# Performance work log

Hardware: AMD Instinct MI355X
Metric: run time of the kernel (lower is better)

The kernel has to match this reference:

```python
import jax, jax.numpy as jnp
import numpy as np

N_HEAD = 8
N_FEAT = 256
CHUNK = 64          # window/chunk size N
D_K = N_FEAT // N_HEAD
SCALE = D_K ** (-0.5)
B_ = 2048           # batch * nChunkNum
NCHUNK = 128        # nChunkNum (B_ % NCHUNK == 0)


def setup_inputs() -> dict:
    key = jax.random.key(0)
    ks = jax.random.split(key, 12)
    f32 = jnp.float32
    query = jax.random.normal(ks[0], (B_, CHUNK, N_FEAT), f32)
    key_t = jax.random.normal(ks[1], (B_, CHUNK, N_FEAT), f32)
    value = jax.random.normal(ks[2], (B_, CHUNK, N_FEAT), f32)
    # padding mask (B_, time2): multiplicative 0/1 floats
    mask = jax.random.randint(ks[3], (B_, CHUNK), 0, 2).astype(f32)
    # shifted-chunk additive mask (nChunkNum, N, N): 0 for neighbors, -100 otherwise
    cm_bin = jax.random.randint(ks[4], (NCHUNK, CHUNK, CHUNK), 0, 2)
    chunk_mask = jnp.where(cm_bin == 1, 0.0, -100.0).astype(f32)
    def lin(k):
        return jax.random.normal(k, (N_FEAT, N_FEAT), f32) * 0.02
    Wq, Wk, Wv, Wo = lin(ks[5]), lin(ks[6]), lin(ks[7]), lin(ks[8])
    bq = jnp.zeros((N_FEAT,), f32)
    bk = jnp.zeros((N_FEAT,), f32)
    bv = jnp.zeros((N_FEAT,), f32)
    bo = jnp.zeros((N_FEAT,), f32)
    rpb_table = jax.random.normal(ks[9], (2 * CHUNK - 1, N_HEAD), f32) * 0.02
    return {"query": query, "key": key_t, "value": value, "mask": mask,
            "chunk_mask": chunk_mask, "Wq": Wq, "bq": bq, "Wk": Wk, "bk": bk,
            "Wv": Wv, "bv": bv, "Wo": Wo, "bo": bo, "rpb_table": rpb_table}


def _rel_pos_index():
    # index[i, j] = (i - j) + CHUNK - 1, shape (N, N)
    w = jnp.arange(CHUNK)
    return w[:, None] - w[None, :] + (CHUNK - 1)


def reference(query, key, value, mask, chunk_mask, Wq, bq, Wk, bk, Wv, bv, Wo, bo, rpb_table):
    B, N, _ = query.shape
    # qkv projections -> (B, h, N, d_k)
    def proj(x, W, b):
        y = x @ W.T + b
        return y.reshape(B, N, N_HEAD, D_K).transpose(0, 2, 1, 3)
    q = proj(query, Wq, bq)
    k = proj(key, Wk, bk)
    v = proj(value, Wv, bv)
    # windowed attention scores (B, h, N, N)
    scores = jnp.einsum("bhid,bhjd->bhij", q, k) * SCALE
    # relative position bias: gather (N, N, h) -> (h, N, N)
    rpb = rpb_table[_rel_pos_index()].transpose(2, 0, 1)
    scores = scores + rpb[None]
    # padding mask: multiply, then fill zeros with -100 (as in torch source)
    scores = scores * mask[:, None, None, :]
    scores = jnp.where(scores == 0, jnp.float32(-100.0), scores)
    # additive shifted-chunk mask
    nC = chunk_mask.shape[0]
    scores = scores.reshape(B // nC, nC, N_HEAD, N, N) + chunk_mask[None, :, None]
    scores = scores.reshape(B, N_HEAD, N, N)
    attn = jax.nn.softmax(scores, axis=-1)
    x = jnp.einsum("bhij,bhjd->bhid", attn, v)          # (B, h, N, d_k)
    x = x.transpose(0, 2, 1, 3).reshape(B, N, N_FEAT)     # (B, N, n_feat)
    return x @ Wo.T + bo
```

## Files before the change

kernel.cpp:

```cpp
#include <hip/hip_runtime.h>
#include <hip/hip_bf16.h>

typedef __bf16 bf16_t;
typedef __bf16 bf16x8 __attribute__((ext_vector_type(8)));
typedef __bf16 bf16x4 __attribute__((ext_vector_type(4)));
typedef float f32x4 __attribute__((ext_vector_type(4)));

#define LDA 264
#define SMEM_BYTES 142560

#define OFF_X   0
#define OFF_K   33792
#define OFF_Q   67584
#define OFF_VT  101376
#define OFF_RPB 138240
#define OFF_MSK 142304

__device__ __forceinline__ void stage_x(const float* __restrict__ src, bf16_t* __restrict__ dst, int tid) {
  const float4* s4 = (const float4*)src;
#pragma unroll
  for (int k = 0; k < 8; ++k) {
    int f = tid + (k << 9);
    float4 v = s4[f];
    int row = f >> 6;
    int col = (f & 63) << 2;
    bf16x4 p;
    p[0] = (bf16_t)v.x; p[1] = (bf16_t)v.y; p[2] = (bf16_t)v.z; p[3] = (bf16_t)v.w;
    *(bf16x4*)(dst + row*LDA + col) = p;
  }
}

__device__ __forceinline__ void gemm_64x32(const bf16_t* __restrict__ A, const bf16_t* __restrict__ W,
                                           int cb, int l15, int g, f32x4 acc[4][2]) {
#pragma unroll
  for (int kt = 0; kt < 8; ++kt) {
    bf16x8 a[4];
#pragma unroll
    for (int mt = 0; mt < 4; ++mt)
      a[mt] = *(const bf16x8*)(A + (mt*16 + l15)*LDA + kt*32 + g*8);
#pragma unroll
    for (int nt = 0; nt < 2; ++nt) {
      bf16x8 bw = *(const bf16x8*)(W + (cb + nt*16 + l15)*256 + kt*32 + g*8);
#pragma unroll
      for (int mt = 0; mt < 4; ++mt)
        acc[mt][nt] = __builtin_amdgcn_mfma_f32_16x16x32_bf16(a[mt], bw, acc[mt][nt], 0, 0, 0);
    }
  }
}

__device__ __forceinline__ void write_frag_rowmajor(bf16_t* __restrict__ dst, const f32x4 acc[4][2],
                                                    float b0, float b1, int cb, int l15, int g) {
#pragma unroll
  for (int mt = 0; mt < 4; ++mt)
#pragma unroll
    for (int nt = 0; nt < 2; ++nt) {
      float bias = nt ? b1 : b0;
#pragma unroll
      for (int r = 0; r < 4; ++r)
        dst[(mt*16 + g*4 + r)*LDA + cb + nt*16 + l15] = (bf16_t)(acc[mt][nt][r] + bias);
    }
}

__global__ __launch_bounds__(512, 2) void chunk_attn_kernel(
    const float* __restrict__ qg, const float* __restrict__ kg, const float* __restrict__ vg,
    const float* __restrict__ maskg, const float* __restrict__ cmg,
    const float* __restrict__ bq, const float* __restrict__ bk, const float* __restrict__ bv,
    const float* __restrict__ bo, const float* __restrict__ rpbg,
    const bf16_t* __restrict__ Wb,
    float* __restrict__ outg) {
  extern __shared__ char sm[];
  bf16_t* sX   = (bf16_t*)(sm + OFF_X);
  bf16_t* sK   = (bf16_t*)(sm + OFF_K);
  bf16_t* sQ   = (bf16_t*)(sm + OFF_Q);
  float*  sRpb = (float*)(sm + OFF_RPB);
  float*  sMask= (float*)(sm + OFF_MSK);

  const int b    = blockIdx.x;
  const int tid  = threadIdx.x;
  const int wave = tid >> 6;
  const int lane = tid & 63;
  const int l15  = lane & 15;
  const int g    = lane >> 4;
  const int cb   = wave << 5;
  bf16_t* sVt = (bf16_t*)(sm + OFF_VT) + wave * (32*72);
  char*   pW  = sm + wave * 8192;

  for (int i = tid; i < 127*8; i += 512) sRpb[i] = rpbg[i];
  if (tid < 64) sMask[tid] = maskg[(b << 6) + tid];
  stage_x(qg + (size_t)b*16384, sX, tid);
  __syncthreads();

  {
    f32x4 acc[4][2] = {};
    gemm_64x32(sX, Wb + 0*65536, cb, l15, g, acc);
    write_frag_rowmajor(sQ, acc, bq[cb + l15], bq[cb + 16 + l15], cb, l15, g);
  }
  __syncthreads();
  stage_x(kg + (size_t)b*16384, sX, tid);
  __syncthreads();
  {
    f32x4 acc[4][2] = {};
    gemm_64x32(sX, Wb + 1*65536, cb, l15, g, acc);
    write_frag_rowmajor(sK, acc, bk[cb + l15], bk[cb + 16 + l15], cb, l15, g);
  }
  __syncthreads();
  stage_x(vg + (size_t)b*16384, sX, tid);
  __syncthreads();
  {
    f32x4 acc[4][2] = {};
    gemm_64x32(sX, Wb + 2*65536, cb, l15, g, acc);
    float b0 = bv[cb + l15], b1 = bv[cb + 16 + l15];
#pragma unroll
    for (int nt = 0; nt < 2; ++nt) {
      float bias = nt ? b1 : b0;
#pragma unroll
      for (int mt = 0; mt < 4; ++mt) {
        bf16x4 p;
#pragma unroll
        for (int r = 0; r < 4; ++r) p[r] = (bf16_t)(acc[mt][nt][r] + bias);
        *(bf16x4*)(sVt + (nt*16 + l15)*72 + mt*16 + g*4) = p;
      }
    }
  }

  f32x4 S[4][4];
  {
    bf16x8 aq[4], bkf[4];
#pragma unroll
    for (int mt = 0; mt < 4; ++mt) aq[mt]  = *(const bf16x8*)(sQ + (mt*16 + l15)*LDA + cb + g*8);
#pragma unroll
    for (int nt = 0; nt < 4; ++nt) bkf[nt] = *(const bf16x8*)(sK + (nt*16 + l15)*LDA + cb + g*8);
    const f32x4 z = {};
#pragma unroll
    for (int mt = 0; mt < 4; ++mt)
#pragma unroll
      for (int nt = 0; nt < 4; ++nt)
        S[mt][nt] = __builtin_amdgcn_mfma_f32_16x16x32_bf16(aq[mt], bkf[nt], z, 0, 0, 0);
  }

  const float* cmb = cmg + ((size_t)(b & 127) << 12);
#pragma unroll
  for (int mt = 0; mt < 4; ++mt) {
#pragma unroll
    for (int nt = 0; nt < 4; ++nt) {
      float mj = sMask[nt*16 + l15];
#pragma unroll
      for (int r = 0; r < 4; ++r) {
        int i = mt*16 + g*4 + r;
        int j = nt*16 + l15;
        float cmv = cmb[(i << 6) + j];
        float s1 = S[mt][nt][r] * 0.17677669529663689f + sRpb[((i - j + 63) << 3) + wave];
        S[mt][nt][r] = (mj != 0.0f) ? (s1 + cmv) : (cmv - 100.0f);
      }
    }
  }

  float rinv[4][4];
#pragma unroll
  for (int mt = 0; mt < 4; ++mt) {
#pragma unroll
    for (int r = 0; r < 4; ++r) {
      float m = fmaxf(fmaxf(S[mt][0][r], S[mt][1][r]), fmaxf(S[mt][2][r], S[mt][3][r]));
      m = fmaxf(m, __shfl_xor(m, 1));
      m = fmaxf(m, __shfl_xor(m, 2));
      m = fmaxf(m, __shfl_xor(m, 4));
      m = fmaxf(m, __shfl_xor(m, 8));
      float sum = 0.0f;
#pragma unroll
      for (int nt = 0; nt < 4; ++nt) {
        float p = __expf(S[mt][nt][r] - m);
        S[mt][nt][r] = p;
        sum += p;
      }
      sum += __shfl_xor(sum, 1);
      sum += __shfl_xor(sum, 2);
      sum += __shfl_xor(sum, 4);
      sum += __shfl_xor(sum, 8);
      rinv[mt][r] = 1.0f / sum;
    }
  }

  __syncthreads();

#pragma unroll
  for (int mt = 0; mt < 4; ++mt)
#pragma unroll
    for (int nt = 0; nt < 4; ++nt)
#pragma unroll
      for (int r = 0; r < 4; ++r) {
        int i = mt*16 + g*4 + r;
        int j = nt*16 + l15;
        int c = j >> 3;
        *(bf16_t*)(pW + i*128 + (((c ^ (i & 7)) << 4) | ((j & 7) << 1))) = (bf16_t)S[mt][nt][r];
      }
  __asm__ volatile("s_waitcnt lgkmcnt(0)" ::: "memory");

  f32x4 Xa[4][2] = {};
#pragma unroll
  for (int kt = 0; kt < 2; ++kt) {
    bf16x8 ap[4];
#pragma unroll
    for (int mt = 0; mt < 4; ++mt) {
      int i = mt*16 + l15;
      int c = kt*4 + g;
      ap[mt] = *(const bf16x8*)(pW + i*128 + ((c ^ (i & 7)) << 4));
    }
#pragma unroll
    for (int nt = 0; nt < 2; ++nt) {
      bf16x8 bvf = *(const bf16x8*)(sVt + (nt*16 + l15)*72 + kt*32 + g*8);
#pragma unroll
      for (int mt = 0; mt < 4; ++mt)
        Xa[mt][nt] = __builtin_amdgcn_mfma_f32_16x16x32_bf16(ap[mt], bvf, Xa[mt][nt], 0, 0, 0);
    }
  }

#pragma unroll
  for (int mt = 0; mt < 4; ++mt)
#pragma unroll
    for (int nt = 0; nt < 2; ++nt)
#pragma unroll
      for (int r = 0; r < 4; ++r)
        sQ[(mt*16 + g*4 + r)*LDA + cb + nt*16 + l15] = (bf16_t)(Xa[mt][nt][r] * rinv[mt][r]);
  __syncthreads();

  {
    f32x4 acc[4][2] = {};
    gemm_64x32(sQ, Wb + 3*65536, cb, l15, g, acc);
    float b0 = bo[cb + l15], b1 = bo[cb + 16 + l15];
    float* ob = outg + (size_t)b * 16384;
#pragma unroll
    for (int mt = 0; mt < 4; ++mt)
#pragma unroll
      for (int nt = 0; nt < 2; ++nt) {
        float bias = nt ? b1 : b0;
#pragma unroll
        for (int r = 0; r < 4; ++r)
          ob[(mt*16 + g*4 + r)*256 + cb + nt*16 + l15] = acc[mt][nt][r] + bias;
      }
  }
}

__global__ void cvt_weights(const float* __restrict__ Wq, const float* __restrict__ Wk,
                            const float* __restrict__ Wv, const float* __restrict__ Wo,
                            bf16_t* __restrict__ dst) {
  int idx = blockIdx.x * 256 + threadIdx.x;
  int which = idx >> 14;
  int off = idx & 16383;
  const float* src = (which == 0) ? Wq : (which == 1) ? Wk : (which == 2) ? Wv : Wo;
  float4 v = ((const float4*)src)[off];
  bf16x4 p;
  p[0] = (bf16_t)v.x; p[1] = (bf16_t)v.y; p[2] = (bf16_t)v.z; p[3] = (bf16_t)v.w;
  *(bf16x4*)(dst + which*65536 + off*4) = p;
}

extern "C" void kernel_launch(void* const* d_in, const int* in_sizes, int n_in,
                              void* d_out, int out_size, void* d_ws, size_t ws_size,
                              hipStream_t stream) {
  (void)in_sizes; (void)n_in; (void)out_size; (void)ws_size;
  const float* qg  = (const float*)d_in[0];
  const float* kg  = (const float*)d_in[1];
  const float* vg  = (const float*)d_in[2];
  const float* mg  = (const float*)d_in[3];
  const float* cmg = (const float*)d_in[4];
  const float* Wq  = (const float*)d_in[5];
  const float* bq  = (const float*)d_in[6];
  const float* Wk  = (const float*)d_in[7];
  const float* bk  = (const float*)d_in[8];
  const float* Wv  = (const float*)d_in[9];
  const float* bv  = (const float*)d_in[10];
  const float* Wo  = (const float*)d_in[11];
  const float* bo  = (const float*)d_in[12];
  const float* rpb = (const float*)d_in[13];
  bf16_t* Wb = (bf16_t*)d_ws;
  float* outg = (float*)d_out;

  hipFuncSetAttribute(reinterpret_cast<const void*>(chunk_attn_kernel),
                      hipFuncAttributeMaxDynamicSharedMemorySize, SMEM_BYTES);
  cvt_weights<<<256, 256, 0, stream>>>(Wq, Wk, Wv, Wo, Wb);
  chunk_attn_kernel<<<2048, 512, SMEM_BYTES, stream>>>(qg, kg, vg, mg, cmg,
      bq, bk, bv, bo, rpb, Wb, outg);
}
```

Measured before the change: 290.9 us.

## Shrink shared memory to 70KB with swizzled tiles and transposed score layout

Replaces padded row-major LDS buffers with two XOR-swizzled 32KB tiles that are reused across stages. This cuts shared memory from about 142KB to about 70KB, and the launch bound is raised to allow 4 blocks per CU. Q and K are staged and projected together. Scores are computed transposed (K·Q^T), so softmax reductions run over lanes with fewer shuffles, and the V projection is deferred until after softmax. The P·V product is done in two halves through a per-wave scratch buffer. The higher occupancy target caps registers per thread and may cause spills, since both Q and K accumulators are live at once.

Result: slower. 420.5 us (+44.5%).

```diff
diff --git a/kernel.cpp b/kernel.cpp
--- a/kernel.cpp
+++ b/kernel.cpp
@@ -6,17 +6,23 @@
 typedef __bf16 bf16x4 __attribute__((ext_vector_type(4)));
 typedef float f32x4 __attribute__((ext_vector_type(4)));
 
-#define LDA 264
-#define SMEM_BYTES 142560
-
-#define OFF_X   0
-#define OFF_K   33792
-#define OFF_Q   67584
-#define OFF_VT  101376
-#define OFF_RPB 138240
-#define OFF_MSK 142304
-
-__device__ __forceinline__ void stage_x(const float* __restrict__ src, bf16_t* __restrict__ dst, int tid) {
+#define OFF_A   0
+#define OFF_B   32768
+#define OFF_RPB 65536
+#define OFF_MSK (65536 + 4096)
+#define SMEM_BYTES (65536 + 4096 + 256)
+
+__device__ __forceinline__ int tile_off(int r, int c) {
+  return (r << 9) + ((((c >> 3) ^ (r & 7)) << 4) | ((c & 7) << 1));
+}
+__device__ __forceinline__ int vt_off(int d, int j) {
+  return (d << 7) + ((((j >> 3) ^ (d & 7)) << 4) | ((j & 7) << 1));
+}
+__device__ __forceinline__ int ps_off(int i, int j) {
+  return (i << 6) + ((((j >> 3) ^ ((i >> 1) & 3)) << 4) | ((j & 7) << 1));
+}
+
+__device__ __forceinline__ void stage_x(const float* __restrict__ src, char* __restrict__ dst, int tid) {
   const float4* s4 = (const float4*)src;
 #pragma unroll
   for (int k = 0; k < 8; ++k) {
@@ -26,18 +32,18 @@
     int col = (f & 63) << 2;
     bf16x4 p;
     p[0] = (bf16_t)v.x; p[1] = (bf16_t)v.y; p[2] = (bf16_t)v.z; p[3] = (bf16_t)v.w;
-    *(bf16x4*)(dst + row*LDA + col) = p;
-  }
-}
-
-__device__ __forceinline__ void gemm_64x32(const bf16_t* __restrict__ A, const bf16_t* __restrict__ W,
-                                           int cb, int l15, int g, f32x4 acc[4][2]) {
+    *(bf16x4*)(dst + tile_off(row, col)) = p;
+  }
+}
+
+__device__ __forceinline__ void gemm_tile(const char* __restrict__ sA, const bf16_t* __restrict__ W,
+                                          int cb, int l15, int g, f32x4 acc[4][2]) {
 #pragma unroll
   for (int kt = 0; kt < 8; ++kt) {
     bf16x8 a[4];
 #pragma unroll
     for (int mt = 0; mt < 4; ++mt)
-      a[mt] = *(const bf16x8*)(A + (mt*16 + l15)*LDA + kt*32 + g*8);
+      a[mt] = *(const bf16x8*)(sA + tile_off(mt*16 + l15, kt*32 + g*8));
 #pragma unroll
     for (int nt = 0; nt < 2; ++nt) {
       bf16x8 bw = *(const bf16x8*)(W + (cb + nt*16 + l15)*256 + kt*32 + g*8);
@@ -48,195 +54,178 @@
   }
 }
 
-__device__ __forceinline__ void write_frag_rowmajor(bf16_t* __restrict__ dst, const f32x4 acc[4][2],
-                                                    float b0, float b1, int cb, int l15, int g) {
-#pragma unroll
-  for (int mt = 0; mt < 4; ++mt)
-#pragma unroll
-    for (int nt = 0; nt < 2; ++nt) {
-      float bias = nt ? b1 : b0;
-#pragma unroll
-      for (int r = 0; r < 4; ++r)
-        dst[(mt*16 + g*4 + r)*LDA + cb + nt*16 + l15] = (bf16_t)(acc[mt][nt][r] + bias);
-    }
-}
-
-__global__ __launch_bounds__(512, 2) void chunk_attn_kernel(
+__global__ __launch_bounds__(512, 4) void chunk_attn_kernel(
     const float* __restrict__ qg, const float* __restrict__ kg, const float* __restrict__ vg,
     const float* __restrict__ maskg, const float* __restrict__ cmg,
     const float* __restrict__ bq, const float* __restrict__ bk, const float* __restrict__ bv,
     const float* __restrict__ bo, const float* __restrict__ rpbg,
-    const bf16_t* __restrict__ Wb,
-    float* __restrict__ outg) {
+    const bf16_t* __restrict__ Wb, float* __restrict__ outg) {
   extern __shared__ char sm[];
-  bf16_t* sX   = (bf16_t*)(sm + OFF_X);
-  bf16_t* sK   = (bf16_t*)(sm + OFF_K);
-  bf16_t* sQ   = (bf16_t*)(sm + OFF_Q);
-  float*  sRpb = (float*)(sm + OFF_RPB);
-  float*  sMask= (float*)(sm + OFF_MSK);
-
-  const int b    = blockIdx.x;
-  const int tid  = threadIdx.x;
-  const int wave = tid >> 6;
-  const int lane = tid & 63;
-  const int l15  = lane & 15;
-  const int g    = lane >> 4;
-  const int cb   = wave << 5;
-  bf16_t* sVt = (bf16_t*)(sm + OFF_VT) + wave * (32*72);
-  char*   pW  = sm + wave * 8192;
-
-  for (int i = tid; i < 127*8; i += 512) sRpb[i] = rpbg[i];
+  char*  bufA  = sm + OFF_A;
+  char*  bufB  = sm + OFF_B;
+  float* sRpb  = (float*)(sm + OFF_RPB);
+  float* sMask = (float*)(sm + OFF_MSK);
+
+  const int b = blockIdx.x, tid = threadIdx.x;
+  const int wave = tid >> 6, lane = tid & 63, l15 = lane & 15, g = lane >> 4;
+  const int cb = wave << 5;
+  char* scr = bufB + (wave << 12);
+
+  for (int i = tid; i < 1016; i += 512) sRpb[i] = rpbg[i];
   if (tid < 64) sMask[tid] = maskg[(b << 6) + tid];
-  stage_x(qg + (size_t)b*16384, sX, tid);
-  __syncthreads();
-
-  {
-    f32x4 acc[4][2] = {};
-    gemm_64x32(sX, Wb + 0*65536, cb, l15, g, acc);
-    write_frag_rowmajor(sQ, acc, bq[cb + l15], bq[cb + 16 + l15], cb, l15, g);
-  }
-  __syncthreads();
-  stage_x(kg + (size_t)b*16384, sX, tid);
-  __syncthreads();
-  {
-    f32x4 acc[4][2] = {};
-    gemm_64x32(sX, Wb + 1*65536, cb, l15, g, acc);
-    write_frag_rowmajor(sK, acc, bk[cb + l15], bk[cb + 16 + l15], cb, l15, g);
-  }
-  __syncthreads();
-  stage_x(vg + (size_t)b*16384, sX, tid);
-  __syncthreads();
-  {
-    f32x4 acc[4][2] = {};
-    gemm_64x32(sX, Wb + 2*65536, cb, l15, g, acc);
-    float b0 = bv[cb + l15], b1 = bv[cb + 16 + l15];
-#pragma unroll
-    for (int nt = 0; nt < 2; ++nt) {
-      float bias = nt ? b1 : b0;
+  stage_x(qg + (size_t)b*16384, bufA, tid);
+  stage_x(kg + (size_t)b*16384, bufB, tid);
+  __syncthreads();
+
+  f32x4 qacc[4][2] = {}, kacc[4][2] = {};
+  gemm_tile(bufA, Wb + 0*65536, cb, l15, g, qacc);
+  gemm_tile(bufB, Wb + 1*65536, cb, l15, g, kacc);
+  __syncthreads();
+
+  {
+    float bq0 = bq[cb+l15], bq1 = bq[cb+16+l15];
+    float bk0 = bk[cb+l15], bk1 = bk[cb+16+l15];
+#pragma unroll
+    for (int mt = 0; mt < 4; ++mt)
+#pragma unroll
+      for (int nt = 0; nt < 2; ++nt)
+#pragma unroll
+        for (int r = 0; r < 4; ++r) {
+          int row = mt*16 + g*4 + r, col = cb + nt*16 + l15;
+          *(bf16_t*)(bufA + tile_off(row, col)) = (bf16_t)(qacc[mt][nt][r] + (nt ? bq1 : bq0));
+          *(bf16_t*)(bufB + tile_off(row, col)) = (bf16_t)(kacc[mt][nt][r] + (nt ? bk1 : bk0));
+        }
+  }
+  __asm__ volatile("s_waitcnt lgkmcnt(0)" ::: "memory");
+
+  f32x4 St[4][4];
+  {
+    bf16x8 ka[4], qb[4];
+#pragma unroll
+    for (int t = 0; t < 4; ++t) {
+      ka[t] = *(const bf16x8*)(bufB + tile_off(t*16 + l15, cb + g*8));
+      qb[t] = *(const bf16x8*)(bufA + tile_off(t*16 + l15, cb + g*8));
+    }
+    const f32x4 z = {};
+#pragma unroll
+    for (int mj = 0; mj < 4; ++mj)
+#pragma unroll
+      for (int ni = 0; ni < 4; ++ni)
+        St[mj][ni] = __builtin_amdgcn_mfma_f32_16x16x32_bf16(ka[mj], qb[ni], z, 0, 0, 0);
+  }
+
+  const float* cmb = cmg + ((size_t)(b & 127) << 12);
+#pragma unroll
+  for (int mj = 0; mj < 4; ++mj)
+#pragma unroll
+    for (int r = 0; r < 4; ++r) {
+      int j = mj*16 + g*4 + r;
+      float mv = sMask[j];
+#pragma unroll
+      for (int ni = 0; ni < 4; ++ni) {
+        int i = ni*16 + l15;
+        float cmv = cmb[(i << 6) + j];
+        float s1 = St[mj][ni][r] * 0.17677669529663689f + sRpb[((i - j + 63) << 3) + wave];
+        St[mj][ni][r] = (mv != 0.0f) ? (s1 + cmv) : (cmv - 100.0f);
+      }
+    }
+
+  float rinv[4];
+#pragma unroll
+  for (int ni = 0; ni < 4; ++ni) {
+    float m = -1e30f;
+#pragma unroll
+    for (int mj = 0; mj < 4; ++mj)
+#pragma unroll
+      for (int r = 0; r < 4; ++r) m = fmaxf(m, St[mj][ni][r]);
+    m = fmaxf(m, __shfl_xor(m, 16));
+    m = fmaxf(m, __shfl_xor(m, 32));
+    float s = 0.0f;
+#pragma unroll
+    for (int mj = 0; mj < 4; ++mj)
+#pragma unroll
+      for (int r = 0; r < 4; ++r) {
+        float p = __expf(St[mj][ni][r] - m);
+        St[mj][ni][r] = p;
+        s += p;
+      }
+    s += __shfl_xor(s, 16);
+    s += __shfl_xor(s, 32);
+    rinv[ni] = 1.0f / s;
+  }
+
+  __syncthreads();
+  stage_x(vg + (size_t)b*16384, bufB, tid);
+  __syncthreads();
+
+  {
+    f32x4 vacc[4][2] = {};
+    gemm_tile(bufB, Wb + 2*65536, cb, l15, g, vacc);
+    float b0 = bv[cb+l15], b1 = bv[cb+16+l15];
+#pragma unroll
+    for (int nt = 0; nt < 2; ++nt)
 #pragma unroll
       for (int mt = 0; mt < 4; ++mt) {
         bf16x4 p;
 #pragma unroll
-        for (int r = 0; r < 4; ++r) p[r] = (bf16_t)(acc[mt][nt][r] + bias);
-        *(bf16x4*)(sVt + (nt*16 + l15)*72 + mt*16 + g*4) = p;
-      }
-    }
-  }
-
-  f32x4 S[4][4];
-  {
-    bf16x8 aq[4], bkf[4];
-#pragma unroll
-    for (int mt = 0; mt < 4; ++mt) aq[mt]  = *(const bf16x8*)(sQ + (mt*16 + l15)*LDA + cb + g*8);
-#pragma unroll
-    for (int nt = 0; nt < 4; ++nt) bkf[nt] = *(const bf16x8*)(sK + (nt*16 + l15)*LDA + cb + g*8);
-    const f32x4 z = {};
+        for (int r = 0; r < 4; ++r) p[r] = (bf16_t)(vacc[mt][nt][r] + (nt ? b1 : b0));
+        *(bf16x4*)(bufA + vt_off(cb + nt*16 + l15, mt*16 + g*4)) = p;
+      }
+  }
+  __syncthreads();
+
+  f32x4 Xa[2][4] = {};
+#pragma unroll
+  for (int h2 = 0; h2 < 2; ++h2) {
+#pragma unroll
+    for (int mj = 2*h2; mj < 2*h2 + 2; ++mj)
+#pragma unroll
+      for (int ni = 0; ni < 4; ++ni) {
+        bf16x4 p;
+#pragma unroll
+        for (int r = 0; r < 4; ++r) p[r] = (bf16_t)St[mj][ni][r];
+        *(bf16x4*)(scr + ps_off(ni*16 + l15, (mj & 1)*16 + g*4)) = p;
+      }
+    __asm__ volatile("s_waitcnt lgkmcnt(0)" ::: "memory");
+    bf16x8 va[2], pb[4];
+#pragma unroll
+    for (int mtd = 0; mtd < 2; ++mtd)
+      va[mtd] = *(const bf16x8*)(bufA + vt_off(cb + mtd*16 + l15, h2*32 + g*8));
+#pragma unroll
+    for (int ni = 0; ni < 4; ++ni)
+      pb[ni] = *(const bf16x8*)(scr + ps_off(ni*16 + l15, g*8));
+#pragma unroll
+    for (int mtd = 0; mtd < 2; ++mtd)
+#pragma unroll
+      for (int ni = 0; ni < 4; ++ni)
+        Xa[mtd][ni] = __builtin_amdgcn_mfma_f32_16x16x32_bf16(va[mtd], pb[ni], Xa[mtd][ni], 0, 0, 0);
+  }
+
+  __syncthreads();
+#pragma unroll
+  for (int mtd = 0; mtd < 2; ++mtd)
+#pragma unroll
+    for (int ni = 0; ni < 4; ++ni)
+#pragma unroll
+      for (int r = 0; r < 4; ++r) {
+        int dloc = mtd*16 + g*4 + r;
+        int i = ni*16 + l15;
+        *(bf16_t*)(bufB + tile_off(i, cb + dloc)) = (bf16_t)(Xa[mtd][ni][r] * rinv[ni]);
+      }
+  __syncthreads();
+
+  {
+    f32x4 acc[4][2] = {};
+    gemm_tile(bufB, Wb + 3*65536, cb, l15, g, acc);
+    float b0 = bo[cb+l15], b1 = bo[cb+16+l15];
+    float* ob = outg + (size_t)b * 16384;
 #pragma unroll
     for (int mt = 0; mt < 4; ++mt)
 #pragma unroll
-      for (int nt = 0; nt < 4; ++nt)
-        S[mt][nt] = __builtin_amdgcn_mfma_f32_16x16x32_bf16(aq[mt], bkf[nt], z, 0, 0, 0);
-  }
-
-  const float* cmb = cmg + ((size_t)(b & 127) << 12);
-#pragma unroll
-  for (int mt = 0; mt < 4; ++mt) {
-#pragma unroll
-    for (int nt = 0; nt < 4; ++nt) {
-      float mj = sMask[nt*16 + l15];
-#pragma unroll
-      for (int r = 0; r < 4; ++r) {
-        int i = mt*16 + g*4 + r;
-        int j = nt*16 + l15;
-        float cmv = cmb[(i << 6) + j];
-        float s1 = S[mt][nt][r] * 0.17677669529663689f + sRpb[((i - j + 63) << 3) + wave];
-        S[mt][nt][r] = (mj != 0.0f) ? (s1 + cmv) : (cmv - 100.0f);
-      }
-    }
-  }
-
-  float rinv[4][4];
-#pragma unroll
-  for (int mt = 0; mt < 4; ++mt) {
-#pragma unroll
-    for (int r = 0; r < 4; ++r) {
-      float m = fmaxf(fmaxf(S[mt][0][r], S[mt][1][r]), fmaxf(S[mt][2][r], S[mt][3][r]));
-      m = fmaxf(m, __shfl_xor(m, 1));
-      m = fmaxf(m, __shfl_xor(m, 2));
-      m = fmaxf(m, __shfl_xor(m, 4));
-      m = fmaxf(m, __shfl_xor(m, 8));
-      float sum = 0.0f;
-#pragma unroll
-      for (int nt = 0; nt < 4; ++nt) {
-        float p = __expf(S[mt][nt][r] - m);
-        S[mt][nt][r] = p;
-        sum += p;
-      }
-      sum += __shfl_xor(sum, 1);
-      sum += __shfl_xor(sum, 2);
-      sum += __shfl_xor(sum, 4);
-      sum += __shfl_xor(sum, 8);
-      rinv[mt][r] = 1.0f / sum;
-    }
-  }
-
-  __syncthreads();
-
-#pragma unroll
-  for (int mt = 0; mt < 4; ++mt)
-#pragma unroll
-    for (int nt = 0; nt < 4; ++nt)
-#pragma unroll
-      for (int r = 0; r < 4; ++r) {
-        int i = mt*16 + g*4 + r;
-        int j = nt*16 + l15;
-        int c = j >> 3;
-        *(bf16_t*)(pW + i*128 + (((c ^ (i & 7)) << 4) | ((j & 7) << 1))) = (bf16_t)S[mt][nt][r];
-      }
-  __asm__ volatile("s_waitcnt lgkmcnt(0)" ::: "memory");
-
-  f32x4 Xa[4][2] = {};
-#pragma unroll
-  for (int kt = 0; kt < 2; ++kt) {
-    bf16x8 ap[4];
-#pragma unroll
-    for (int mt = 0; mt < 4; ++mt) {
-      int i = mt*16 + l15;
-      int c = kt*4 + g;
-      ap[mt] = *(const bf16x8*)(pW + i*128 + ((c ^ (i & 7)) << 4));
-    }
-#pragma unroll
-    for (int nt = 0; nt < 2; ++nt) {
-      bf16x8 bvf = *(const bf16x8*)(sVt + (nt*16 + l15)*72 + kt*32 + g*8);
-#pragma unroll
-      for (int mt = 0; mt < 4; ++mt)
-        Xa[mt][nt] = __builtin_amdgcn_mfma_f32_16x16x32_bf16(ap[mt], bvf, Xa[mt][nt], 0, 0, 0);
-    }
-  }
-
-#pragma unroll
-  for (int mt = 0; mt < 4; ++mt)
-#pragma unroll
-    for (int nt = 0; nt < 2; ++nt)
-#pragma unroll
-      for (int r = 0; r < 4; ++r)
-        sQ[(mt*16 + g*4 + r)*LDA + cb + nt*16 + l15] = (bf16_t)(Xa[mt][nt][r] * rinv[mt][r]);
-  __syncthreads();
-
-  {
-    f32x4 acc[4][2] = {};
-    gemm_64x32(sQ, Wb + 3*65536, cb, l15, g, acc);
-    float b0 = bo[cb + l15], b1 = bo[cb + 16 + l15];
-    float* ob = outg + (size_t)b * 16384;
-#pragma unroll
-    for (int mt = 0; mt < 4; ++mt)
-#pragma unroll
-      for (int nt = 0; nt < 2; ++nt) {
-        float bias = nt ? b1 : b0;
+      for (int nt = 0; nt < 2; ++nt)
 #pragma unroll
         for (int r = 0; r < 4; ++r)
-          ob[(mt*16 + g*4 + r)*256 + cb + nt*16 + l15] = acc[mt][nt][r] + bias;
-      }
+          ob[(mt*16 + g*4 + r)*256 + cb + nt*16 + l15] = acc[mt][nt][r] + (nt ? b1 : b0);
   }
 }
 
```
